# Kernel tuning notes

Measured on AMD Instinct MI355X. Metric: run time of the kernel, lower is better.

## Reference

```python
import jax, jax.numpy as jnp
from jax import lax
import numpy as np
import math

B, L = 32, 2048
HID = int(max(8.0 * (1.0 + math.log(L)), 64.0))   # 68
DIN = 2 * HID                                      # expand=2 -> 136
DST, DCV = 16, 4                                   # d_state, d_conv
DTR = math.ceil(HID / 16)                          # dt_rank = 5
OUT = 128                                          # len(list_data)


def _p(k, shape, s=0.02):
    return jax.random.normal(k, shape, jnp.float32) * s


def setup_inputs() -> dict:
    key = jax.random.key(0)
    ks = iter(jax.random.split(key, 40))
    d = {"ipt": jax.random.normal(next(ks), (B, L, 3), jnp.float32)}
    d["W0"] = _p(next(ks), (HID, 3)); d["b0"] = jnp.zeros((HID,), jnp.float32)
    for i in range(2):
        p = f"m{i}_"
        d[p + "in_w"] = _p(next(ks), (2 * DIN, HID))
        d[p + "conv_w"] = _p(next(ks), (DIN, DCV), 0.1)
        d[p + "conv_b"] = jnp.zeros((DIN,), jnp.float32)
        d[p + "x_w"] = _p(next(ks), (DTR + 2 * DST, DIN))
        d[p + "dt_w"] = _p(next(ks), (DIN, DTR), 0.1)
        d[p + "dt_b"] = jnp.full((DIN,), -4.0, jnp.float32)  # softplus -> small dt
        d[p + "A_log"] = jnp.log(jnp.broadcast_to(jnp.arange(1, DST + 1, dtype=jnp.float32), (DIN, DST)))
        d[p + "D"] = jnp.ones((DIN,), jnp.float32)
        d[p + "out_w"] = _p(next(ks), (HID, DIN))
        d[f"l{i}_w"] = _p(next(ks), (HID, HID))
        d[f"l{i}_b"] = jnp.zeros((HID,), jnp.float32)
    d["W1"] = _p(next(ks), (OUT, HID)); d["b1"] = jnp.zeros((OUT,), jnp.float32)
    return d


def mamba_block(x, in_w, conv_w, conv_b, x_w, dt_w, dt_b, A_log, Dp, out_w):
    # x: [B, L, HID]
    b, l, _ = x.shape
    xz = x @ in_w.T                                  # [B, L, 2*DIN]
    xi, z = jnp.split(xz, 2, axis=-1)
    # causal depthwise conv1d over time
    xp = jnp.pad(xi, ((0, 0), (DCV - 1, 0), (0, 0))).transpose(0, 2, 1)  # [B, DIN, L+DCV-1]
    xi = lax.conv_general_dilated(xp, conv_w[:, None, :], (1,), 'VALID',
                                  feature_group_count=DIN,
                                  dimension_numbers=('NCH', 'OIH', 'NCH'))
    xi = jax.nn.silu(xi.transpose(0, 2, 1) + conv_b)  # [B, L, DIN]
    x_dbl = xi @ x_w.T                                # [B, L, DTR+2*DST]
    dt, Bm, Cm = jnp.split(x_dbl, [DTR, DTR + DST], axis=-1)
    delta = jax.nn.softplus(dt @ dt_w.T + dt_b)       # [B, L, DIN]
    A = -jnp.exp(A_log)                               # [DIN, DST]

    def step(h, inp):
        d_t, B_t, C_t, x_t = inp                      # [B,DIN],[B,DST],[B,DST],[B,DIN]
        dA = jnp.exp(d_t[..., None] * A)              # [B, DIN, DST]
        h = dA * h + (d_t * x_t)[..., None] * B_t[:, None, :]
        y = jnp.einsum('bdn,bn->bd', h, C_t)
        return h, y

    h0 = jnp.zeros((b, DIN, DST), x.dtype)
    xs = (delta.transpose(1, 0, 2), Bm.transpose(1, 0, 2), Cm.transpose(1, 0, 2), xi.transpose(1, 0, 2))
    _, ys = lax.scan(step, h0, xs)                    # ys: [L, B, DIN]
    y = ys.transpose(1, 0, 2) + xi * Dp
    y = y * jax.nn.silu(z)
    return y @ out_w.T                                # [B, L, HID]


def reference(ipt, W0, b0,
              m0_in_w, m0_conv_w, m0_conv_b, m0_x_w, m0_dt_w, m0_dt_b, m0_A_log, m0_D, m0_out_w,
              l0_w, l0_b,
              m1_in_w, m1_conv_w, m1_conv_b, m1_x_w, m1_dt_w, m1_dt_b, m1_A_log, m1_D, m1_out_w,
              l1_w, l1_b, W1, b1):
    tnf = 1.0 / (L / 12.0)
    x = jnp.stack([ipt[:, :, 0] / 127.0,
                   ipt[:, :, 1] / tnf,
                   jnp.zeros_like(ipt[:, :, 0])], axis=-1)  # channel 2 stays zero
    h = x @ W0.T + b0
    # block 0 (Dropout is identity at inference)
    h = jax.nn.sigmoid(h)
    h = mamba_block(h, m0_in_w, m0_conv_w, m0_conv_b, m0_x_w, m0_dt_w, m0_dt_b, m0_A_log, m0_D, m0_out_w)
    h = jax.nn.sigmoid(h)
    h = h @ l0_w.T + l0_b
    # block 1
    h = jax.nn.sigmoid(h)
    h = mamba_block(h, m1_in_w, m1_conv_w, m1_conv_b, m1_x_w, m1_dt_w, m1_dt_b, m1_A_log, m1_D, m1_out_w)
    h = jax.nn.sigmoid(h)
    h = h @ l1_w.T + l1_b
    out = h[:, -1, :] @ W1.T + b1                     # [B, OUT]
    return jax.nn.softmax(out, axis=1)
```

## Files before the change

kernel.cpp:

```cpp
#include <hip/hip_runtime.h>


#define BB 32
#define SEQ 2048
#define HID 68
#define DIN 136
#define DIN2 272
#define DST 16
#define DTR 5
#define NOUT 128
#define NROW (BB * SEQ)
#define NCH 64
#define LCH 32
#define BCDW 40

__device__ __forceinline__ float sigm(float x) { return 1.f / (1.f + __expf(-x)); }

struct TransDesc { const float* s; float* d; int n; int k; };
struct TransArgs { TransDesc t[8]; };

__global__ void transpose_all(TransArgs a) {
    TransDesc td = a.t[blockIdx.x];
    int total = td.n * td.k;
    for (int i = threadIdx.x; i < total; i += 256) {
        int r = i / td.k;
        int c = i - r * td.k;
        td.d[c * td.n + r] = td.s[i];
    }
}

__global__ void xw_pack(const float* __restrict__ xw0, const float* __restrict__ xw1,
                        float* __restrict__ d0, float* __restrict__ d1) {
    const float* s = blockIdx.x ? xw1 : xw0;
    float* d = blockIdx.x ? d1 : d0;
    for (int i = threadIdx.x; i < 136 * 40; i += 256) {
        int k = i / 40, j = i - k * 40;
        int m = (j < 5) ? j : ((j < 8) ? -1 : j - 3);
        d[i] = (m >= 0) ? s[m * 136 + k] : 0.f;
    }
}

__global__ void front_kernel(const float* __restrict__ ipt, const float* __restrict__ W0,
                             const float* __restrict__ b0, float* __restrict__ HS) {
    int flat = blockIdx.x * 256 + threadIdx.x;
    int row = flat / HID;
    int j = flat - row * HID;
    float x0 = ipt[row * 3 + 0] * (1.f / 127.f);
    float x1 = ipt[row * 3 + 1] * ((float)SEQ / 12.f);
    float h = x0 * W0[j * 3 + 0] + x1 * W0[j * 3 + 1] + b0[j];
    HS[flat] = sigm(h);
}

template <int K, int NT, int RPT, bool OSIG, bool BIAS>
__launch_bounds__(128, 3)
__global__ void gemm_lds(const float* __restrict__ A, const float* __restrict__ WT,
                         const float* __restrict__ bias, float* __restrict__ Out, int N) {
    constexpr int NTP = ((NT + 3) / 4) * 4;
    __shared__ float wlds[K][NTP];
    const int tid = threadIdx.x;
    const long rowbase = (long)blockIdx.x * (128 * RPT);
    const int jbase = blockIdx.y * NT;
    for (int i = tid; i < K * NT; i += 128) {
        int k = i / NT;
        int j = i - k * NT;
        wlds[k][j] = WT[(size_t)k * N + jbase + j];
    }
    __syncthreads();
    float acc[RPT][NT];
#pragma unroll
    for (int r = 0; r < RPT; ++r)
#pragma unroll
        for (int j = 0; j < NT; ++j) acc[r][j] = 0.f;
    const float* ar0 = A + (rowbase + tid) * K;
    for (int k4 = 0; k4 < K / 4; ++k4) {
        float4 a[RPT];
#pragma unroll
        for (int r = 0; r < RPT; ++r) a[r] = *(const float4*)(ar0 + (size_t)r * 128 * K + k4 * 4);
#pragma unroll
        for (int kk = 0; kk < 4; ++kk) {
            int k = k4 * 4 + kk;
            float w[NT];
#pragma unroll
            for (int q = 0; q < NT / 4; ++q) *(float4*)(w + 4 * q) = *(const float4*)(&wlds[k][4 * q]);
#pragma unroll
            for (int j = (NT / 4) * 4; j < NT; ++j) w[j] = wlds[k][j];
#pragma unroll
            for (int r = 0; r < RPT; ++r) {
                float av = ((const float*)(&a[r]))[kk];
#pragma unroll
                for (int j = 0; j < NT; ++j) acc[r][j] = fmaf(av, w[j], acc[r][j]);
            }
        }
    }
#pragma unroll
    for (int r = 0; r < RPT; ++r) {
        float* orow = Out + (rowbase + tid + (size_t)r * 128) * N + jbase;
#pragma unroll
        for (int j = 0; j < NT; ++j) {
            float v = acc[r][j];
            if (BIAS) v += bias[jbase + j];
            if (OSIG) v = sigm(v);
            orow[j] = v;
        }
    }
}

__launch_bounds__(256)
__global__ void xproj_tile(const float* __restrict__ XZ, const float* __restrict__ cw,
                           const float* __restrict__ cb, const float* __restrict__ XWB,
                           float* __restrict__ BCD) {
    __shared__ float At[34][260];
    __shared__ float Wt[136][44];
    const int tid = threadIdx.x;
    const int tx = tid & 7, ty = tid >> 3;
    const long rowbase = (long)blockIdx.x * 256;
    for (int i = tid; i < 136 * 40; i += 256) {
        int k = i / 40, j = i - k * 40;
        Wt[k][j] = XWB[i];
    }
    float4 acc[8];
    float accs[8];
#pragma unroll
    for (int r = 0; r < 8; ++r) { acc[r] = make_float4(0.f, 0.f, 0.f, 0.f); accs[r] = 0.f; }
    for (int p = 0; p < 4; ++p) {
        const int kt = p * 34;
        __syncthreads();
        for (int i = tid; i < 256 * 34; i += 256) {
            int r = i / 34, k = i - r * 34;
            int kc = kt + k;
            long g = rowbase + r;
            int t = (int)(g & (SEQ - 1));
            const float* xp = XZ + g * DIN2 + kc;
            float x3 = xp[0];
            float x2 = (t >= 1) ? xp[-DIN2] : 0.f;
            float x1 = (t >= 2) ? xp[-2 * DIN2] : 0.f;
            float x0 = (t >= 3) ? xp[-3 * DIN2] : 0.f;
            float4 c4 = *(const float4*)(cw + kc * 4);
            float v = cb[kc];
            v = fmaf(x0, c4.x, v); v = fmaf(x1, c4.y, v);
            v = fmaf(x2, c4.z, v); v = fmaf(x3, c4.w, v);
            At[k][r] = v * sigm(v);
        }
        __syncthreads();
#pragma unroll 2
        for (int k = 0; k < 34; ++k) {
            float ar[8];
            *(float4*)&ar[0] = *(const float4*)&At[k][8 * ty];
            *(float4*)&ar[4] = *(const float4*)&At[k][8 * ty + 4];
            float4 w = *(const float4*)&Wt[kt + k][4 * tx];
            float wsg = Wt[kt + k][32 + tx];
#pragma unroll
            for (int r = 0; r < 8; ++r) {
                float av = ar[r];
                acc[r].x = fmaf(av, w.x, acc[r].x);
                acc[r].y = fmaf(av, w.y, acc[r].y);
                acc[r].z = fmaf(av, w.z, acc[r].z);
                acc[r].w = fmaf(av, w.w, acc[r].w);
                accs[r] = fmaf(av, wsg, accs[r]);
            }
        }
    }
#pragma unroll
    for (int r = 0; r < 8; ++r) {
        long row = rowbase + 8 * ty + r;
        float* o = BCD + row * BCDW;
        *(float4*)(o + 4 * tx) = acc[r];
        o[32 + tx] = accs[r];
    }
}

__launch_bounds__(192)
__global__ void scanA_kernel(const float* __restrict__ XZ, const float* __restrict__ BCD,
                             const float* __restrict__ cw, const float* __restrict__ cb,
                             const float* __restrict__ dtw, const float* __restrict__ dtb,
                             float* __restrict__ Sb, float* __restrict__ Q) {
    __shared__ float bcd[LCH][BCDW];
    const int tid = threadIdx.x;
    const int c = blockIdx.x, b = blockIdx.y;
    const int rowbase = b * SEQ + c * LCH;
    const float4* src = (const float4*)(BCD + (size_t)rowbase * BCDW);
    float4* dstl = (float4*)&bcd[0][0];
    for (int i = tid; i < LCH * BCDW / 4; i += 192) dstl[i] = src[i];
    __syncthreads();
    if (tid >= DIN) return;
    const int d = tid;
    const float4 c4 = *(const float4*)(cw + d * 4);
    const float cbd = cb[d];
    const float w0 = dtw[d * 5 + 0], w1 = dtw[d * 5 + 1], w2 = dtw[d * 5 + 2],
                w3 = dtw[d * 5 + 3], w4 = dtw[d * 5 + 4];
    const float dtbd = dtb[d];
    const float* xz = XZ + (size_t)rowbase * DIN2 + d;
    float xm3 = (c > 0) ? xz[-3 * DIN2] : 0.f;
    float xm2 = (c > 0) ? xz[-2 * DIN2] : 0.f;
    float xm1 = (c > 0) ? xz[-DIN2] : 0.f;
    float xcur = xz[0];
    float h[DST];
#pragma unroll
    for (int n = 0; n < DST; ++n) h[n] = 0.f;
    float S = 0.f;
    for (int t = 0; t < LCH; ++t) {
        float xnext = (t < LCH - 1) ? xz[(t + 1) * DIN2] : 0.f;
        float v = cbd;
        v = fmaf(xm3, c4.x, v); v = fmaf(xm2, c4.y, v);
        v = fmaf(xm1, c4.z, v); v = fmaf(xcur, c4.w, v);
        float xv = v * sigm(v);
        float4 q5 = *(const float4*)&bcd[t][0];
        float dl = dtbd;
        dl = fmaf(q5.x, w0, dl); dl = fmaf(q5.y, w1, dl);
        dl = fmaf(q5.z, w2, dl); dl = fmaf(q5.w, w3, dl);
        dl = fmaf(bcd[t][4], w4, dl);
        dl = (dl > 20.f) ? dl : __logf(1.f + __expf(dl));
        float r = __expf(-dl);
        float dx = dl * xv;
        float Bv[16];
        ((float4*)Bv)[0] = *(const float4*)&bcd[t][8];
        ((float4*)Bv)[1] = *(const float4*)&bcd[t][12];
        ((float4*)Bv)[2] = *(const float4*)&bcd[t][16];
        ((float4*)Bv)[3] = *(const float4*)&bcd[t][20];
        float p = r;
#pragma unroll
        for (int n = 0; n < DST; ++n) { h[n] = fmaf(p, h[n], dx * Bv[n]); p *= r; }
        S += dl;
        xm3 = xm2; xm2 = xm1; xm1 = xcur; xcur = xnext;
    }
    int qb = (b * NCH + c) * DIN + d;
    Sb[qb] = S;
    float4* qp = (float4*)(Q + (size_t)qb * 16);
    qp[0] = make_float4(h[0], h[1], h[2], h[3]);
    qp[1] = make_float4(h[4], h[5], h[6], h[7]);
    qp[2] = make_float4(h[8], h[9], h[10], h[11]);
    qp[3] = make_float4(h[12], h[13], h[14], h[15]);
}

__launch_bounds__(256)
__global__ void scanB_kernel(const float* __restrict__ Sb, const float* __restrict__ Q,
                             float* __restrict__ HI) {
    int flat = blockIdx.x * 256 + threadIdx.x;
    int n = flat & 15;
    int bd = flat >> 4;
    int b = bd / DIN;
    int d = bd - b * DIN;
    float h = 0.f;
    float nf = -(float)(n + 1);
    for (int c = 0; c < NCH; ++c) {
        int base = (b * NCH + c) * DIN + d;
        HI[(size_t)base * 16 + n] = h;
        float S = Sb[base];
        float P = __expf(nf * S);
        h = fmaf(P, h, Q[(size_t)base * 16 + n]);
    }
}

template <bool LAST_ONLY>
__launch_bounds__(192)
__global__ void scanC_kernel(const float* __restrict__ XZ, const float* __restrict__ BCD,
                             const float* __restrict__ cw, const float* __restrict__ cb,
                             const float* __restrict__ dtw, const float* __restrict__ dtb,
                             const float* __restrict__ HI, const float* __restrict__ Dw,
                             float* __restrict__ Yo) {
    __shared__ float bcd[LCH][BCDW];
    const int tid = threadIdx.x;
    const int c = LAST_ONLY ? (NCH - 1) : blockIdx.x;
    const int b = blockIdx.y;
    const int rowbase = b * SEQ + c * LCH;
    const float4* src = (const float4*)(BCD + (size_t)rowbase * BCDW);
    float4* dstl = (float4*)&bcd[0][0];
    for (int i = tid; i < LCH * BCDW / 4; i += 192) dstl[i] = src[i];
    __syncthreads();
    if (tid >= DIN) return;
    const int d = tid;
    const float4 c4 = *(const float4*)(cw + d * 4);
    const float cbd = cb[d];
    const float w0 = dtw[d * 5 + 0], w1 = dtw[d * 5 + 1], w2 = dtw[d * 5 + 2],
                w3 = dtw[d * 5 + 3], w4 = dtw[d * 5 + 4];
    const float dtbd = dtb[d];
    const int qb = (b * NCH + c) * DIN + d;
    const float4* hi4 = (const float4*)(HI + (size_t)qb * 16);
    float h[16];
    ((float4*)h)[0] = hi4[0];
    ((float4*)h)[1] = hi4[1];
    ((float4*)h)[2] = hi4[2];
    ((float4*)h)[3] = hi4[3];
    float Dv = Dw[d];
    const float* xz = XZ + (size_t)rowbase * DIN2 + d;
    const float* zp = XZ + (size_t)rowbase * DIN2 + DIN + d;
    float xm3 = (c > 0) ? xz[-3 * DIN2] : 0.f;
    float xm2 = (c > 0) ? xz[-2 * DIN2] : 0.f;
    float xm1 = (c > 0) ? xz[-DIN2] : 0.f;
    float xcur = xz[0];
    float zcur = zp[0];
    float* yo = Yo + (size_t)rowbase * DIN + d;
    for (int t = 0; t < LCH; ++t) {
        float xnext = (t < LCH - 1) ? xz[(t + 1) * DIN2] : 0.f;
        float znext = (t < LCH - 1) ? zp[(t + 1) * DIN2] : 0.f;
        float v = cbd;
        v = fmaf(xm3, c4.x, v); v = fmaf(xm2, c4.y, v);
        v = fmaf(xm1, c4.z, v); v = fmaf(xcur, c4.w, v);
        float xv = v * sigm(v);
        float4 q5 = *(const float4*)&bcd[t][0];
        float dl = dtbd;
        dl = fmaf(q5.x, w0, dl); dl = fmaf(q5.y, w1, dl);
        dl = fmaf(q5.z, w2, dl); dl = fmaf(q5.w, w3, dl);
        dl = fmaf(bcd[t][4], w4, dl);
        dl = (dl > 20.f) ? dl : __logf(1.f + __expf(dl));
        float r = __expf(-dl);
        float dx = dl * xv;
        float p = r;
        float ya = 0.f, yb = 0.f, yc = 0.f, yd = 0.f;
#pragma unroll
        for (int n = 0; n < 16; n += 4) {
            h[n + 0] = fmaf(p, h[n + 0], dx * bcd[t][8 + n + 0]); ya = fmaf(h[n + 0], bcd[t][24 + n + 0], ya); p *= r;
            h[n + 1] = fmaf(p, h[n + 1], dx * bcd[t][8 + n + 1]); yb = fmaf(h[n + 1], bcd[t][24 + n + 1], yb); p *= r;
            h[n + 2] = fmaf(p, h[n + 2], dx * bcd[t][8 + n + 2]); yc = fmaf(h[n + 2], bcd[t][24 + n + 2], yc); p *= r;
            h[n + 3] = fmaf(p, h[n + 3], dx * bcd[t][8 + n + 3]); yd = fmaf(h[n + 3], bcd[t][24 + n + 3], yd); p *= r;
        }
        float y = ((ya + yb) + (yc + yd)) + xv * Dv;
        float sg = zcur * sigm(zcur);
        float outv = y * sg;
        if (!LAST_ONLY) {
            yo[t * DIN] = outv;
        } else if (t == LCH - 1) {
            Yo[b * DIN + d] = outv;
        }
        xm3 = xm2; xm2 = xm1; xm1 = xcur; xcur = xnext;
        zcur = znext;
    }
}

__launch_bounds__(128)
__global__ void tail_kernel(const float* __restrict__ YL, const float* __restrict__ OWT,
                            const float* __restrict__ LWT, const float* __restrict__ lb,
                            const float* __restrict__ W1, const float* __restrict__ b1,
                            float* __restrict__ out) {
    __shared__ float yl[DIN], sm[HID], gg[HID], red[4];
    int b = blockIdx.x, tid = threadIdx.x;
    for (int i = tid; i < DIN; i += 128) yl[i] = YL[b * DIN + i];
    __syncthreads();
    if (tid < HID) {
        float m = 0.f;
        for (int dd = 0; dd < DIN; ++dd) m = fmaf(yl[dd], OWT[dd * HID + tid], m);
        sm[tid] = sigm(m);
    }
    __syncthreads();
    if (tid < HID) {
        float g = lb[tid];
        for (int j = 0; j < HID; ++j) g = fmaf(sm[j], LWT[j * HID + tid], g);
        gg[tid] = g;
    }
    __syncthreads();
    float lo = b1[tid];
    for (int j = 0; j < HID; ++j) lo = fmaf(gg[j], W1[tid * HID + j], lo);
    float mx = lo;
    for (int o = 32; o > 0; o >>= 1) mx = fmaxf(mx, __shfl_xor(mx, o, 64));
    if ((tid & 63) == 0) red[tid >> 6] = mx;
    __syncthreads();
    float gmx = fmaxf(red[0], red[1]);
    float e = __expf(lo - gmx);
    float s = e;
    for (int o = 32; o > 0; o >>= 1) s += __shfl_xor(s, o, 64);
    if ((tid & 63) == 0) red[2 + (tid >> 6)] = s;
    __syncthreads();
    float ts = red[2] + red[3];
    out[b * NOUT + tid] = e / ts;
}

extern "C" void kernel_launch(void* const* d_in, const int* in_sizes, int n_in,
                              void* d_out, int out_size, void* d_ws, size_t ws_size,
                              hipStream_t stream) {
    const float* ipt = (const float*)d_in[0];
    const float* W0 = (const float*)d_in[1];
    const float* b0 = (const float*)d_in[2];
    const float* m_in_w[2]   = {(const float*)d_in[3],  (const float*)d_in[14]};
    const float* m_conv_w[2] = {(const float*)d_in[4],  (const float*)d_in[15]};
    const float* m_conv_b[2] = {(const float*)d_in[5],  (const float*)d_in[16]};
    const float* m_x_w[2]    = {(const float*)d_in[6],  (const float*)d_in[17]};
    const float* m_dt_w[2]   = {(const float*)d_in[7],  (const float*)d_in[18]};
    const float* m_dt_b[2]   = {(const float*)d_in[8],  (const float*)d_in[19]};
    const float* m_D[2]      = {(const float*)d_in[10], (const float*)d_in[21]};
    const float* m_out_w[2]  = {(const float*)d_in[11], (const float*)d_in[22]};
    const float* l_w[2]      = {(const float*)d_in[12], (const float*)d_in[23]};
    const float* l_b[2]      = {(const float*)d_in[13], (const float*)d_in[24]};
    const float* W1 = (const float*)d_in[25];
    const float* b1 = (const float*)d_in[26];

    float* ws = (float*)d_ws;
    const size_t O_XZ  = 0;
    const size_t O_BCD = O_XZ  + (size_t)NROW * DIN2;
    const size_t O_HS  = O_BCD + (size_t)NROW * BCDW;
    const size_t O_G0  = O_HS  + (size_t)NROW * HID;
    const size_t O_Y   = O_G0  + (size_t)NROW * HID;
    const size_t O_S   = O_Y   + (size_t)NROW * DIN;
    const size_t O_Q   = O_S   + (size_t)BB * NCH * DIN;
    const size_t O_HI  = O_Q   + (size_t)BB * NCH * DIN * DST;
    const size_t O_YL  = O_HI  + (size_t)BB * NCH * DIN * DST;
    const size_t O_WT  = O_YL  + (size_t)BB * DIN;

    float* XZ  = ws + O_XZ;
    float* BCD = ws + O_BCD;
    float* HS  = ws + O_HS;
    float* G0  = ws + O_G0;
    float* Yb  = ws + O_Y;
    float* Sb  = ws + O_S;
    float* Qb  = ws + O_Q;
    float* HIb = ws + O_HI;
    float* YL  = ws + O_YL;
    float* WTb = ws + O_WT;

    const size_t WBLK = 37808;
    TransArgs ta;
    for (int blk = 0; blk < 2; ++blk) {
        float* base = WTb + blk * WBLK;
        ta.t[blk * 3 + 0] = {m_in_w[blk],  base + 0,     DIN2, HID};
        ta.t[blk * 3 + 1] = {m_out_w[blk], base + 18496, HID,  DIN};
        ta.t[blk * 3 + 2] = {l_w[blk],     base + 27744, HID,  HID};
    }
    ta.t[6] = ta.t[0]; ta.t[7] = ta.t[0];
    transpose_all<<<6, 256, 0, stream>>>(ta);
    xw_pack<<<2, 256, 0, stream>>>(m_x_w[0], m_x_w[1], WTb + 32368, WTb + WBLK + 32368);

    front_kernel<<<(NROW * HID) / 256, 256, 0, stream>>>(ipt, W0, b0, HS);

    for (int blk = 0; blk < 2; ++blk) {
        const float* WT_in  = WTb + blk * WBLK + 0;
        const float* WT_out = WTb + blk * WBLK + 18496;
        const float* WT_l   = WTb + blk * WBLK + 27744;
        const float* XWB    = WTb + blk * WBLK + 32368;

        gemm_lds<HID, 16, 4, false, false><<<dim3(128, 17), 128, 0, stream>>>(
            blk == 0 ? HS : G0, WT_in, nullptr, XZ, DIN2);

        xproj_tile<<<NROW / 256, 256, 0, stream>>>(XZ, m_conv_w[blk], m_conv_b[blk], XWB, BCD);

        scanA_kernel<<<dim3(NCH, BB), 192, 0, stream>>>(XZ, BCD, m_conv_w[blk], m_conv_b[blk],
                                                        m_dt_w[blk], m_dt_b[blk], Sb, Qb);
        scanB_kernel<<<(BB * DIN * DST) / 256, 256, 0, stream>>>(Sb, Qb, HIb);

        if (blk == 0) {
            scanC_kernel<false><<<dim3(NCH, BB), 192, 0, stream>>>(XZ, BCD, m_conv_w[blk], m_conv_b[blk],
                                                                   m_dt_w[blk], m_dt_b[blk], HIb, m_D[0], Yb);
            gemm_lds<DIN, 17, 4, true, false><<<dim3(128, 4), 128, 0, stream>>>(
                Yb, WT_out, nullptr, HS, HID);
            gemm_lds<HID, 17, 4, true, true><<<dim3(128, 4), 128, 0, stream>>>(
                HS, WT_l, l_b[0], G0, HID);
        } else {
            scanC_kernel<true><<<dim3(1, BB), 192, 0, stream>>>(XZ, BCD, m_conv_w[blk], m_conv_b[blk],
                                                                m_dt_w[blk], m_dt_b[blk], HIb, m_D[1], YL);
            tail_kernel<<<BB, 128, 0, stream>>>(YL, WT_out, WT_l, l_b[1], W1, b1, (float*)d_out);
        }
    }
}
```

Baseline: 726.0 us.

## Store in_proj GEMM input transposed and add register-tiled GEMM for it

The front kernel and the last linear layer of block 0 now write their activations feature-major (transposed), so a new in_proj GEMM kernel can read contiguous float4 rows across sequence positions and write float4 output rows. Each thread computes 8 rows by 16 columns, which raises register reuse compared with the old per-row strided loads. The out_proj and l0 GEMMs switch to 2 rows per thread with twice as many blocks, and the launch_bounds occupancy hint is dropped. The transposed store in the l0 GEMM is strided per thread, which could add write cost, and the larger accumulator set raises register pressure.

```diff
diff --git a/kernel.cpp b/kernel.cpp
--- a/kernel.cpp
+++ b/kernel.cpp
@@ -41,18 +41,70 @@
 }
 
 __global__ void front_kernel(const float* __restrict__ ipt, const float* __restrict__ W0,
-                             const float* __restrict__ b0, float* __restrict__ HS) {
+                             const float* __restrict__ b0, float* __restrict__ HST) {
     int flat = blockIdx.x * 256 + threadIdx.x;
-    int row = flat / HID;
-    int j = flat - row * HID;
+    int j = flat >> 16;
+    int row = flat & (NROW - 1);
     float x0 = ipt[row * 3 + 0] * (1.f / 127.f);
     float x1 = ipt[row * 3 + 1] * ((float)SEQ / 12.f);
     float h = x0 * W0[j * 3 + 0] + x1 * W0[j * 3 + 1] + b0[j];
-    HS[flat] = sigm(h);
-}
-
-template <int K, int NT, int RPT, bool OSIG, bool BIAS>
+    HST[flat] = sigm(h);
+}
+
 __launch_bounds__(128, 3)
+__global__ void gemm_inT(const float* __restrict__ AT, const float* __restrict__ WT,
+                         float* __restrict__ Out) {
+    __shared__ float wlds[HID][16];
+    const int tid = threadIdx.x;
+    const int jbase = blockIdx.x * 16;
+    const long rbase = (long)blockIdx.y * 1024;
+    for (int i = tid; i < HID * 16; i += 128) {
+        int k = i >> 4, j = i & 15;
+        wlds[k][j] = WT[k * DIN2 + jbase + j];
+    }
+    __syncthreads();
+    float acc[2][4][16];
+#pragma unroll
+    for (int i = 0; i < 2; ++i)
+#pragma unroll
+        for (int u = 0; u < 4; ++u)
+#pragma unroll
+            for (int j = 0; j < 16; ++j) acc[i][u][j] = 0.f;
+    const float* a0 = AT + rbase + 4 * tid;
+#pragma unroll 2
+    for (int k = 0; k < HID; ++k) {
+        float4 a[2];
+        a[0] = *(const float4*)(a0 + (size_t)k * NROW);
+        a[1] = *(const float4*)(a0 + (size_t)k * NROW + 512);
+        float w[16];
+#pragma unroll
+        for (int q = 0; q < 4; ++q) *(float4*)(w + 4 * q) = *(const float4*)&wlds[k][4 * q];
+#pragma unroll
+        for (int i = 0; i < 2; ++i) {
+            float au[4];
+            *(float4*)au = a[i];
+#pragma unroll
+            for (int u = 0; u < 4; ++u)
+#pragma unroll
+                for (int j = 0; j < 16; ++j)
+                    acc[i][u][j] = fmaf(au[u], w[j], acc[i][u][j]);
+        }
+    }
+#pragma unroll
+    for (int i = 0; i < 2; ++i)
+#pragma unroll
+        for (int u = 0; u < 4; ++u) {
+            long r = rbase + 4 * tid + u + i * 512;
+            float* orow = Out + r * DIN2 + jbase;
+#pragma unroll
+            for (int q = 0; q < 4; ++q)
+                *(float4*)(orow + 4 * q) = make_float4(acc[i][u][4 * q], acc[i][u][4 * q + 1],
+                                                      acc[i][u][4 * q + 2], acc[i][u][4 * q + 3]);
+        }
+}
+
+template <int K, int NT, int RPT, bool OSIG, bool BIAS, bool OUTT>
+__launch_bounds__(128)
 __global__ void gemm_lds(const float* __restrict__ A, const float* __restrict__ WT,
                          const float* __restrict__ bias, float* __restrict__ Out, int N) {
     constexpr int NTP = ((NT + 3) / 4) * 4;
@@ -94,13 +146,16 @@
     }
 #pragma unroll
     for (int r = 0; r < RPT; ++r) {
-        float* orow = Out + (rowbase + tid + (size_t)r * 128) * N + jbase;
+        float* orow = OUTT ? nullptr : (Out + (rowbase + tid + (size_t)r * 128) * N + jbase);
 #pragma unroll
         for (int j = 0; j < NT; ++j) {
             float v = acc[r][j];
             if (BIAS) v += bias[jbase + j];
             if (OSIG) v = sigm(v);
-            orow[j] = v;
+            if (OUTT)
+                Out[(size_t)(jbase + j) * NROW + rowbase + tid + (size_t)r * 128] = v;
+            else
+                orow[j] = v;
         }
     }
 }
@@ -386,9 +441,10 @@
     float* ws = (float*)d_ws;
     const size_t O_XZ  = 0;
     const size_t O_BCD = O_XZ  + (size_t)NROW * DIN2;
-    const size_t O_HS  = O_BCD + (size_t)NROW * BCDW;
-    const size_t O_G0  = O_HS  + (size_t)NROW * HID;
-    const size_t O_Y   = O_G0  + (size_t)NROW * HID;
+    const size_t O_HST = O_BCD + (size_t)NROW * BCDW;
+    const size_t O_G0T = O_HST + (size_t)NROW * HID;
+    const size_t O_HS  = O_G0T + (size_t)NROW * HID;
+    const size_t O_Y   = O_HS  + (size_t)NROW * HID;
     const size_t O_S   = O_Y   + (size_t)NROW * DIN;
     const size_t O_Q   = O_S   + (size_t)BB * NCH * DIN;
     const size_t O_HI  = O_Q   + (size_t)BB * NCH * DIN * DST;
@@ -397,8 +453,9 @@
 
     float* XZ  = ws + O_XZ;
     float* BCD = ws + O_BCD;
+    float* HST = ws + O_HST;
+    float* G0T = ws + O_G0T;
     float* HS  = ws + O_HS;
-    float* G0  = ws + O_G0;
     float* Yb  = ws + O_Y;
     float* Sb  = ws + O_S;
     float* Qb  = ws + O_Q;
@@ -418,7 +475,7 @@
     transpose_all<<<6, 256, 0, stream>>>(ta);
     xw_pack<<<2, 256, 0, stream>>>(m_x_w[0], m_x_w[1], WTb + 32368, WTb + WBLK + 32368);
 
-    front_kernel<<<(NROW * HID) / 256, 256, 0, stream>>>(ipt, W0, b0, HS);
+    front_kernel<<<(NROW * HID) / 256, 256, 0, stream>>>(ipt, W0, b0, HST);
 
     for (int blk = 0; blk < 2; ++blk) {
         const float* WT_in  = WTb + blk * WBLK + 0;
@@ -426,8 +483,7 @@
         const float* WT_l   = WTb + blk * WBLK + 27744;
         const float* XWB    = WTb + blk * WBLK + 32368;
 
-        gemm_lds<HID, 16, 4, false, false><<<dim3(128, 17), 128, 0, stream>>>(
-            blk == 0 ? HS : G0, WT_in, nullptr, XZ, DIN2);
+        gemm_inT<<<dim3(17, 64), 128, 0, stream>>>(blk == 0 ? HST : G0T, WT_in, XZ);
 
         xproj_tile<<<NROW / 256, 256, 0, stream>>>(XZ, m_conv_w[blk], m_conv_b[blk], XWB, BCD);
 
@@ -438,10 +494,10 @@
         if (blk == 0) {
             scanC_kernel<false><<<dim3(NCH, BB), 192, 0, stream>>>(XZ, BCD, m_conv_w[blk], m_conv_b[blk],
                                                                    m_dt_w[blk], m_dt_b[blk], HIb, m_D[0], Yb);
-            gemm_lds<DIN, 17, 4, true, false><<<dim3(128, 4), 128, 0, stream>>>(
+            gemm_lds<DIN, 17, 2, true, false, false><<<dim3(256, 4), 128, 0, stream>>>(
                 Yb, WT_out, nullptr, HS, HID);
-            gemm_lds<HID, 17, 4, true, true><<<dim3(128, 4), 128, 0, stream>>>(
-                HS, WT_l, l_b[0], G0, HID);
+            gemm_lds<HID, 17, 2, true, true, true><<<dim3(256, 4), 128, 0, stream>>>(
+                HS, WT_l, l_b[0], G0T, HID);
         } else {
             scanC_kernel<true><<<dim3(1, BB), 192, 0, stream>>>(XZ, BCD, m_conv_w[blk], m_conv_b[blk],
                                                                 m_dt_w[blk], m_dt_b[blk], HIb, m_D[1], YL);
```

New measurement: 644.7 us. 1.13x faster.
